# Kernel tuning notes

Hardware: AMD Instinct MI355X
Metric: run time of the kernel (lower is better)

Reference implementation:

```python
import jax, jax.numpy as jnp
import numpy as np

DN = ('NCHW', 'OIHW', 'NCHW')


def conv2d(x, w, b, pad=1):
    y = jax.lax.conv_general_dilated(x, w, window_strides=(1, 1),
                                     padding=[(pad, pad), (pad, pad)],
                                     dimension_numbers=DN)
    return y + b[None, :, None, None]


def deform_conv2d(x, offset, w, b):
    """Deformable conv v1 (torchvision layout): offset [B, 2*K*K, H, W],
    channel 2k = dy_k, 2k+1 = dx_k, kernel points row-major."""
    B, C, H, W = x.shape
    K = 3
    off = offset.reshape(B, K * K, 2, H, W)
    dy, dx = off[:, :, 0], off[:, :, 1]            # [B,9,H,W]
    ky = jnp.repeat(jnp.arange(K) - 1, K).astype(x.dtype)   # row-major kernel grid
    kx = jnp.tile(jnp.arange(K) - 1, K).astype(x.dtype)
    hh = jnp.arange(H, dtype=x.dtype)
    ww = jnp.arange(W, dtype=x.dtype)
    py = hh[None, None, :, None] + ky[None, :, None, None] + dy  # [B,9,H,W]
    px = ww[None, None, None, :] + kx[None, :, None, None] + dx

    y0 = jnp.floor(py)
    x0 = jnp.floor(px)
    ly, lx = py - y0, px - x0
    y0i, x0i = y0.astype(jnp.int32), x0.astype(jnp.int32)

    def gather(yi, xi):
        valid = ((yi >= 0) & (yi < H) & (xi >= 0) & (xi < W))
        yc = jnp.clip(yi, 0, H - 1)
        xc = jnp.clip(xi, 0, W - 1)
        # per-batch fancy gather: [C,H,W] indexed by [9,H,W] -> [C,9,H,W]
        g = jax.vmap(lambda xb, yy, xx: xb[:, yy, xx])(x, yc, xc)  # [B,C,9,H,W]
        return g * valid[:, None].astype(x.dtype)

    w00 = ((1 - ly) * (1 - lx))[:, None]
    w01 = ((1 - ly) * lx)[:, None]
    w10 = (ly * (1 - lx))[:, None]
    w11 = (ly * lx)[:, None]
    val = (gather(y0i, x0i) * w00 + gather(y0i, x0i + 1) * w01 +
           gather(y0i + 1, x0i) * w10 + gather(y0i + 1, x0i + 1) * w11)  # [B,C,9,H,W]

    wk = w.reshape(w.shape[0], C * K * K)                 # [Cout, C*9]
    out = jnp.einsum('bkhw,ok->bohw', val.reshape(B, C * K * K, H, W), wk)
    return out + b[None, :, None, None]


def setup_inputs() -> dict:
    key = jax.random.key(0)
    k1, k2, k3, k4 = jax.random.split(key, 4)
    B, Cin, Cout, H, W = 8, 128, 256, 64, 64
    fan = 1.0 / np.sqrt(Cin * 9)
    return {
        'x': jax.random.normal(k1, (B, Cin, H, W), jnp.float32),
        'w_off': jax.random.normal(k2, (18, Cin, 3, 3), jnp.float32) * 0.01,
        'b_off': jnp.zeros((18,), jnp.float32),
        'w_def': jax.random.normal(k3, (Cout, Cin, 3, 3), jnp.float32) * fan,
        'b_def': jax.random.normal(k4, (Cout,), jnp.float32) * 0.01,
    }


def reference(x, w_off, b_off, w_def, b_def):
    offset = conv2d(x, w_off, b_off, pad=1)
    y = deform_conv2d(x, offset, w_def, b_def)
    return jax.nn.relu(y)
```

## Files before the change

### kernel.cpp

```cpp
#include <hip/hip_runtime.h>
#include <hip/hip_bf16.h>

#define HH 64
#define WW 64
#define CIN 128
#define COUT 256
#define KK 1152
#define TP 32
#define PW 66
#define XTIMG (PW*PW*CIN)

typedef short bf16x8 __attribute__((ext_vector_type(8)));
typedef float f32x4  __attribute__((ext_vector_type(4)));

__device__ inline short f2bf(float f) {
    union { float f; unsigned u; } v; v.f = f;
    unsigned r = v.u + 0x7FFFu + ((v.u >> 16) & 1u);
    return (short)(r >> 16);
}
__device__ inline float bf2f(ushort u) {
    union { unsigned u; float f; } v; v.u = (unsigned)u << 16; return v.f;
}

__global__ __launch_bounds__(256) void transpose_x(const float* __restrict__ x,
                                                   ushort* __restrict__ xt) {
    __shared__ short tl[64][130];
    int hp = blockIdx.x;
    int b  = blockIdx.y;
    int t  = threadIdx.x;
    ushort* row = xt + ((size_t)b * PW + hp) * PW * CIN;
    if (hp == 0 || hp == PW - 1) {
        for (int i = 0; i < 33; i++) row[i * 256 + t] = 0;
        return;
    }
    int h = hp - 1;
    int w = t & 63, cq = t >> 6;
    for (int it = 0; it < 32; it++) {
        int c = it * 4 + cq;
        tl[w][c] = f2bf(x[(((size_t)b * CIN + c) << 12) + (h << 6) + w]);
    }
    __syncthreads();
    for (int it = 0; it < 33; it++) {
        int flat = it * 256 + t;
        int wp = flat >> 7, c = flat & 127;
        ushort v = (wp == 0 || wp == PW - 1) ? (ushort)0 : (ushort)tl[wp - 1][c];
        row[flat] = v;
    }
}

__global__ void cast_wf(const float* __restrict__ wd, short* __restrict__ wf) {
    int ks = blockIdx.x, m = blockIdx.y, l = threadIdx.x;
    int co = m * 16 + (l & 15);
    bf16x8 v;
#pragma unroll
    for (int j = 0; j < 8; j++) {
        int ckp = ks * 32 + ((l >> 4) << 3) + j;
        int c = ckp & 127, k = ckp >> 7;
        v[j] = f2bf(wd[(size_t)co * KK + c * 9 + k]);
    }
    *(bf16x8*)(wf + ((size_t)(m * 36 + ks) * 64 + l) * 8) = v;
}

__global__ void cast_wfo(const float* __restrict__ w, short* __restrict__ wfo) {
    int ks = blockIdx.x, m = blockIdx.y, l = threadIdx.x;
    int co = m * 16 + (l & 15);
    bf16x8 v;
#pragma unroll
    for (int j = 0; j < 8; j++) {
        int ckp = ks * 32 + ((l >> 4) << 3) + j;
        int c = ckp & 127, k = ckp >> 7;
        v[j] = (co < 18) ? f2bf(w[(size_t)co * KK + c * 9 + k]) : (short)0;
    }
    *(bf16x8*)(wfo + ((size_t)(m * 36 + ks) * 64 + l) * 8) = v;
}

__global__ __launch_bounds__(256, 4) void off_mfma(const ushort* __restrict__ xt,
                                                   const short* __restrict__ wfo,
                                                   const float* __restrict__ bo,
                                                   float* __restrict__ off) {
    __shared__ short s_val[2][TP][128];

    int t = threadIdx.x, bi = blockIdx.x;
    int b = bi & 7, h = (bi >> 3) & 63, tile = bi >> 9, w0 = tile * TP;
    const ushort* xb = xt + (size_t)b * XTIMG;

    bf16x8 r0, r1;
    int cpix = t >> 3;
    int g0 = ((2 * t) & 15), g1 = g0 + 1;
    int gs0 = (g0 ^ (cpix & 15)) * 8, gs1 = (g1 ^ (cpix & 15)) * 8;

    auto oload = [&](int k) {
        const ushort* base = xb + ((size_t)(h + k / 3) * PW + w0 + k % 3) * CIN;
        r0 = *(const bf16x8*)(base + t * 16);
        r1 = *(const bf16x8*)(base + t * 16 + 8);
    };
    auto ostore = [&](int buf) {
        *(bf16x8*)&s_val[buf][cpix][gs0] = r0;
        *(bf16x8*)&s_val[buf][cpix][gs1] = r1;
    };

    int wv = t >> 6, l = t & 63, lane16 = l & 15, quad = l >> 4;
    int mt = wv >> 1, nt = wv & 1;
    f32x4 acc = {0.f, 0.f, 0.f, 0.f};
    const short* Ab = wfo + (size_t)l * 8 + (size_t)mt * 36 * 512;

    oload(0); ostore(0);
    __syncthreads();
    for (int k = 0; k < 9; k++) {
        if (k < 8) oload(k + 1);
#pragma unroll
        for (int ksp = 0; ksp < 4; ksp++) {
            int ks = k * 4 + ksp;
            bf16x8 a  = *(const bf16x8*)(Ab + ks * 512);
            bf16x8 bf = *(const bf16x8*)&s_val[k & 1][nt * 16 + lane16][((ksp * 4 + quad) ^ lane16) * 8];
            acc = __builtin_amdgcn_mfma_f32_16x16x32_bf16(a, bf, acc, 0, 0, 0);
        }
        if (k < 8) ostore((k + 1) & 1);
        __syncthreads();
    }
    int cob = mt * 16 + quad * 4;
#pragma unroll
    for (int r = 0; r < 4; r++) {
        int co = cob + r;
        if (co < 18)
            off[(((size_t)b * 18 + co) << 12) + (h << 6) + w0 + nt * 16 + lane16] = acc[r] + bo[co];
    }
}

__global__ __launch_bounds__(256, 4) void deform_mfma(const ushort* __restrict__ xt,
                                                      const float* __restrict__ off,
                                                      const short* __restrict__ wf,
                                                      const float* __restrict__ bias,
                                                      float* __restrict__ out) {
    __shared__ float4  s_w[9][TP];
    __shared__ ushort2 s_o[9][TP];
    __shared__ short   s_val[2][TP][128];

    int t = threadIdx.x, bi = blockIdx.x;
    int b = bi & 7, h = (bi >> 3) & 63, tile = bi >> 9, w0 = tile * TP;

    for (int jj = t; jj < 9 * TP; jj += 256) {
        int k = jj >> 5, pixj = jj & 31, wp = w0 + pixj;
        float dy = off[(((size_t)b * 18 + 2 * k    ) << 12) + (h << 6) + wp];
        float dx = off[(((size_t)b * 18 + 2 * k + 1) << 12) + (h << 6) + wp];
        float py = (float)(h + k / 3 - 1) + dy;
        float px = (float)(wp + k % 3 - 1) + dx;
        float y0f = floorf(py), x0f = floorf(px);
        float ly = py - y0f, lx = px - x0f;
        int y0 = (int)y0f, x0 = (int)x0f;
        float a0, a1;
        if (x0 >= 0 && x0 <= 62)      { a0 = 1.f - lx; a1 = lx; }
        else if (x0 == -1)            { a0 = lx;       a1 = 0.f; }
        else if (x0 == 63)            { a0 = 0.f;      a1 = 1.f - lx; }
        else                          { a0 = 0.f;      a1 = 0.f; }
        int xb0 = min(max(x0, 0), 62);
        bool vy0 = (y0 >= 0) && (y0 < HH);
        bool vy1 = (y0 >= -1) && (y0 < HH - 1);
        int y0c = min(max(y0, 0), HH - 1);
        int y1c = min(max(y0 + 1, 0), HH - 1);
        float wy0 = (1.f - ly) * (vy0 ? 1.f : 0.f);
        float wy1 = ly * (vy1 ? 1.f : 0.f);
        s_o[k][pixj] = make_ushort2((ushort)((y0c + 1) * PW + xb0 + 1),
                                    (ushort)((y1c + 1) * PW + xb0 + 1));
        s_w[k][pixj] = make_float4(wy0 * a0, wy0 * a1, wy1 * a0, wy1 * a1);
    }
    __syncthreads();

    int pix = t & 31, cs = t >> 5, pm = pix & 15;
    const ushort* xb = xt + (size_t)b * XTIMG;
    int gs0 = ((cs * 2) ^ pm) * 8, gs1 = ((cs * 2 + 1) ^ pm) * 8;

    bf16x8 r[8];
    auto gload = [&](int k) {
        ushort2 o = s_o[k][pix];
        const ushort* p0 = xb + (size_t)o.x * CIN + cs * 16;
        const ushort* p1 = xb + (size_t)o.y * CIN + cs * 16;
        r[0] = *(const bf16x8*)(p0);       r[1] = *(const bf16x8*)(p0 + 8);
        r[2] = *(const bf16x8*)(p0 + 128); r[3] = *(const bf16x8*)(p0 + 136);
        r[4] = *(const bf16x8*)(p1);       r[5] = *(const bf16x8*)(p1 + 8);
        r[6] = *(const bf16x8*)(p1 + 128); r[7] = *(const bf16x8*)(p1 + 136);
    };
    auto gstore = [&](int k, int buf) {
        float4 w4 = s_w[k][pix];
        bf16x8 va, vb;
#pragma unroll
        for (int j = 0; j < 8; j++) {
            float v = w4.x * bf2f((ushort)r[0][j]) + w4.y * bf2f((ushort)r[2][j])
                    + w4.z * bf2f((ushort)r[4][j]) + w4.w * bf2f((ushort)r[6][j]);
            float u = w4.x * bf2f((ushort)r[1][j]) + w4.y * bf2f((ushort)r[3][j])
                    + w4.z * bf2f((ushort)r[5][j]) + w4.w * bf2f((ushort)r[7][j]);
            va[j] = f2bf(v);
            vb[j] = f2bf(u);
        }
        *(bf16x8*)&s_val[buf][pix][gs0] = va;
        *(bf16x8*)&s_val[buf][pix][gs1] = vb;
    };

    int wv = t >> 6, l = t & 63, lane16 = l & 15, quad = l >> 4;
    f32x4 z = {0.f, 0.f, 0.f, 0.f};
    f32x4 acc[4][2];
#pragma unroll
    for (int i = 0; i < 4; i++)
#pragma unroll
        for (int j = 0; j < 2; j++) acc[i][j] = z;

    const short* Ab = wf + (size_t)l * 8 + (size_t)(wv * 4) * 36 * 512;

    gload(0); gstore(0, 0);
    __syncthreads();
    for (int k = 0; k < 9; k++) {
        if (k < 8) gload(k + 1);
#pragma unroll
        for (int ksp = 0; ksp < 4; ksp++) {
            int ks = k * 4 + ksp;
            bf16x8 a0 = *(const bf16x8*)(Ab + (0 * 36 + ks) * 512);
            bf16x8 a1 = *(const bf16x8*)(Ab + (1 * 36 + ks) * 512);
            bf16x8 a2 = *(const bf16x8*)(Ab + (2 * 36 + ks) * 512);
            bf16x8 a3 = *(const bf16x8*)(Ab + (3 * 36 + ks) * 512);
            int gsw = ((ksp * 4 + quad) ^ lane16) * 8;
            bf16x8 b0 = *(const bf16x8*)&s_val[k & 1][lane16     ][gsw];
            bf16x8 b1 = *(const bf16x8*)&s_val[k & 1][16 + lane16][gsw];
            acc[0][0] = __builtin_amdgcn_mfma_f32_16x16x32_bf16(a0, b0, acc[0][0], 0, 0, 0);
            acc[1][0] = __builtin_amdgcn_mfma_f32_16x16x32_bf16(a1, b0, acc[1][0], 0, 0, 0);
            acc[2][0] = __builtin_amdgcn_mfma_f32_16x16x32_bf16(a2, b0, acc[2][0], 0, 0, 0);
            acc[3][0] = __builtin_amdgcn_mfma_f32_16x16x32_bf16(a3, b0, acc[3][0], 0, 0, 0);
            acc[0][1] = __builtin_amdgcn_mfma_f32_16x16x32_bf16(a0, b1, acc[0][1], 0, 0, 0);
            acc[1][1] = __builtin_amdgcn_mfma_f32_16x16x32_bf16(a1, b1, acc[1][1], 0, 0, 0);
            acc[2][1] = __builtin_amdgcn_mfma_f32_16x16x32_bf16(a2, b1, acc[2][1], 0, 0, 0);
            acc[3][1] = __builtin_amdgcn_mfma_f32_16x16x32_bf16(a3, b1, acc[3][1], 0, 0, 0);
        }
        if (k < 8) gstore(k + 1, (k + 1) & 1);
        __syncthreads();
    }

#pragma unroll
    for (int ct = 0; ct < 4; ct++) {
        int co = wv * 64 + ct * 16 + quad * 4;
#pragma unroll
        for (int pt = 0; pt < 2; pt++) {
            int colx = w0 + pt * 16 + lane16;
#pragma unroll
            for (int rr = 0; rr < 4; rr++) {
                float v = acc[ct][pt][rr] + bias[co + rr];
                out[(((size_t)b * COUT + co + rr) << 12) + (h << 6) + colx] = fmaxf(v, 0.f);
            }
        }
    }
}

extern "C" void kernel_launch(void* const* d_in, const int* in_sizes, int n_in,
                              void* d_out, int out_size, void* d_ws, size_t ws_size,
                              hipStream_t stream) {
    const float* x     = (const float*)d_in[0];
    const float* w_off = (const float*)d_in[1];
    const float* b_off = (const float*)d_in[2];
    const float* w_def = (const float*)d_in[3];
    const float* b_def = (const float*)d_in[4];
    float* out = (float*)d_out;

    float*  offset = (float*)d_ws;
    short*  wf     = (short*)(offset + (size_t)8 * 18 * HH * WW);
    short*  wfo    = wf + (size_t)16 * 36 * 512;
    ushort* xt     = (ushort*)(wfo + (size_t)2 * 36 * 512);

    transpose_x<<<dim3(PW, 8), 256, 0, stream>>>(x, xt);
    cast_wf<<<dim3(36, 16), 64, 0, stream>>>(w_def, wf);
    cast_wfo<<<dim3(36, 2), 64, 0, stream>>>(w_off, wfo);
    off_mfma<<<1024, 256, 0, stream>>>(xt, wfo, b_off, offset);
    deform_mfma<<<1024, 256, 0, stream>>>(xt, offset, wf, b_def, out);
}
```

Baseline: 147.7 us.

## Fuse offset conv into deform kernel, restage gathers via LDS, vectorize transpose

The offset convolution and the deformable conv now run in one kernel: offsets go to shared memory instead of global, and the two weight cast kernels merge into one launch. The deform gather is reorganised so that 4 threads load one corner row into a raw LDS buffer, and a separate combine pass does the bilinear blend. The transpose kernel uses float4 loads and ushort4 stores. This removes the offset round-trip through global memory and two launches. In exchange it uses much more LDS (occupancy bound drops to 3), adds extra barriers per k step, and drops the double-buffering of the value tile.

```diff
diff --git a/kernel.cpp b/kernel.cpp
--- a/kernel.cpp
+++ b/kernel.cpp
@@ -9,6 +9,7 @@
 #define TP 32
 #define PW 66
 #define XTIMG (PW*PW*CIN)
+#define RS 264
 
 typedef short bf16x8 __attribute__((ext_vector_type(8)));
 typedef float f32x4  __attribute__((ext_vector_type(4)));
@@ -24,125 +25,129 @@
 
 __global__ __launch_bounds__(256) void transpose_x(const float* __restrict__ x,
                                                    ushort* __restrict__ xt) {
-    __shared__ short tl[64][130];
     int hp = blockIdx.x;
     int b  = blockIdx.y;
     int t  = threadIdx.x;
     ushort* row = xt + ((size_t)b * PW + hp) * PW * CIN;
     if (hp == 0 || hp == PW - 1) {
-        for (int i = 0; i < 33; i++) row[i * 256 + t] = 0;
+        ushort4 z4 = {0, 0, 0, 0};
+        for (int f = t; f < 2112; f += 256) ((ushort4*)row)[f] = z4;
         return;
     }
+    __shared__ short tl[66 * 132];
     int h = hp - 1;
-    int w = t & 63, cq = t >> 6;
-    for (int it = 0; it < 32; it++) {
-        int c = it * 4 + cq;
-        tl[w][c] = f2bf(x[(((size_t)b * CIN + c) << 12) + (h << 6) + w]);
-    }
-    __syncthreads();
-    for (int it = 0; it < 33; it++) {
-        int flat = it * 256 + t;
-        int wp = flat >> 7, c = flat & 127;
-        ushort v = (wp == 0 || wp == PW - 1) ? (ushort)0 : (ushort)tl[wp - 1][c];
-        row[flat] = v;
-    }
-}
-
-__global__ void cast_wf(const float* __restrict__ wd, short* __restrict__ wf) {
+    if (t < 128) { tl[t] = 0; tl[65 * 132 + t] = 0; }
+    const float* xbh = x + (((size_t)b * CIN) << 12) + (h << 6);
+#pragma unroll
+    for (int it = 0; it < 8; it++) {
+        int c  = it * 16 + (t >> 4);
+        int w4 = (t & 15) * 4;
+        float4 v = *(const float4*)(xbh + ((size_t)c << 12) + w4);
+        tl[(w4 + 1) * 132 + c] = f2bf(v.x);
+        tl[(w4 + 2) * 132 + c] = f2bf(v.y);
+        tl[(w4 + 3) * 132 + c] = f2bf(v.z);
+        tl[(w4 + 4) * 132 + c] = f2bf(v.w);
+    }
+    __syncthreads();
+    for (int f = t; f < 2112; f += 256) {
+        int wp = f >> 5, c4 = (f & 31) * 4;
+        const short* s = &tl[wp * 132 + c4];
+        ushort4 v; v.x = s[0]; v.y = s[1]; v.z = s[2]; v.w = s[3];
+        ((ushort4*)row)[f] = v;
+    }
+}
+
+__global__ void cast_wall(const float* __restrict__ wd, const float* __restrict__ wo,
+                          short* __restrict__ wf, short* __restrict__ wfo) {
     int ks = blockIdx.x, m = blockIdx.y, l = threadIdx.x;
-    int co = m * 16 + (l & 15);
     bf16x8 v;
-#pragma unroll
-    for (int j = 0; j < 8; j++) {
-        int ckp = ks * 32 + ((l >> 4) << 3) + j;
-        int c = ckp & 127, k = ckp >> 7;
-        v[j] = f2bf(wd[(size_t)co * KK + c * 9 + k]);
-    }
-    *(bf16x8*)(wf + ((size_t)(m * 36 + ks) * 64 + l) * 8) = v;
-}
-
-__global__ void cast_wfo(const float* __restrict__ w, short* __restrict__ wfo) {
-    int ks = blockIdx.x, m = blockIdx.y, l = threadIdx.x;
-    int co = m * 16 + (l & 15);
-    bf16x8 v;
-#pragma unroll
-    for (int j = 0; j < 8; j++) {
-        int ckp = ks * 32 + ((l >> 4) << 3) + j;
-        int c = ckp & 127, k = ckp >> 7;
-        v[j] = (co < 18) ? f2bf(w[(size_t)co * KK + c * 9 + k]) : (short)0;
-    }
-    *(bf16x8*)(wfo + ((size_t)(m * 36 + ks) * 64 + l) * 8) = v;
-}
-
-__global__ __launch_bounds__(256, 4) void off_mfma(const ushort* __restrict__ xt,
-                                                   const short* __restrict__ wfo,
-                                                   const float* __restrict__ bo,
-                                                   float* __restrict__ off) {
-    __shared__ short s_val[2][TP][128];
+    if (m < 16) {
+        int co = m * 16 + (l & 15);
+#pragma unroll
+        for (int j = 0; j < 8; j++) {
+            int ckp = ks * 32 + ((l >> 4) << 3) + j;
+            int c = ckp & 127, k = ckp >> 7;
+            v[j] = f2bf(wd[(size_t)co * KK + c * 9 + k]);
+        }
+        *(bf16x8*)(wf + ((size_t)(m * 36 + ks) * 64 + l) * 8) = v;
+    } else {
+        int mm = m - 16;
+        int co = mm * 16 + (l & 15);
+#pragma unroll
+        for (int j = 0; j < 8; j++) {
+            int ckp = ks * 32 + ((l >> 4) << 3) + j;
+            int c = ckp & 127, k = ckp >> 7;
+            v[j] = (co < 18) ? f2bf(wo[(size_t)co * KK + c * 9 + k]) : (short)0;
+        }
+        *(bf16x8*)(wfo + ((size_t)(mm * 36 + ks) * 64 + l) * 8) = v;
+    }
+}
+
+__global__ __launch_bounds__(256, 3) void fused_deform(const ushort* __restrict__ xt,
+                                                       const short* __restrict__ wf,
+                                                       const short* __restrict__ wfo,
+                                                       const float* __restrict__ bo,
+                                                       const float* __restrict__ bias,
+                                                       float* __restrict__ out) {
+    __shared__ short   s_raw[64 * RS];
+    __shared__ short   s_val[TP][128];
+    __shared__ float   s_off[18][TP];
+    __shared__ float4  s_w[9][TP];
+    __shared__ ushort2 s_o[9][TP];
 
     int t = threadIdx.x, bi = blockIdx.x;
     int b = bi & 7, h = (bi >> 3) & 63, tile = bi >> 9, w0 = tile * TP;
     const ushort* xb = xt + (size_t)b * XTIMG;
-
-    bf16x8 r0, r1;
-    int cpix = t >> 3;
-    int g0 = ((2 * t) & 15), g1 = g0 + 1;
-    int gs0 = (g0 ^ (cpix & 15)) * 8, gs1 = (g1 ^ (cpix & 15)) * 8;
-
-    auto oload = [&](int k) {
-        const ushort* base = xb + ((size_t)(h + k / 3) * PW + w0 + k % 3) * CIN;
-        r0 = *(const bf16x8*)(base + t * 16);
-        r1 = *(const bf16x8*)(base + t * 16 + 8);
-    };
-    auto ostore = [&](int buf) {
-        *(bf16x8*)&s_val[buf][cpix][gs0] = r0;
-        *(bf16x8*)&s_val[buf][cpix][gs1] = r1;
-    };
-
     int wv = t >> 6, l = t & 63, lane16 = l & 15, quad = l >> 4;
-    int mt = wv >> 1, nt = wv & 1;
-    f32x4 acc = {0.f, 0.f, 0.f, 0.f};
-    const short* Ab = wfo + (size_t)l * 8 + (size_t)mt * 36 * 512;
-
-    oload(0); ostore(0);
-    __syncthreads();
-    for (int k = 0; k < 9; k++) {
-        if (k < 8) oload(k + 1);
-#pragma unroll
-        for (int ksp = 0; ksp < 4; ksp++) {
-            int ks = k * 4 + ksp;
-            bf16x8 a  = *(const bf16x8*)(Ab + ks * 512);
-            bf16x8 bf = *(const bf16x8*)&s_val[k & 1][nt * 16 + lane16][((ksp * 4 + quad) ^ lane16) * 8];
-            acc = __builtin_amdgcn_mfma_f32_16x16x32_bf16(a, bf, acc, 0, 0, 0);
-        }
-        if (k < 8) ostore((k + 1) & 1);
+
+    {
+        short* sv0 = s_raw;
+        short* sv1 = s_raw + 4096;
+        int cpix = t >> 3;
+        int g0 = 2 * (t & 7), g1 = g0 + 1;
+        int gs0 = (g0 ^ (cpix & 15)) * 8, gs1 = (g1 ^ (cpix & 15)) * 8;
+        bf16x8 r0, r1;
+        auto oload = [&](int k) {
+            const ushort* base = xb + ((size_t)(h + k / 3) * PW + w0 + k % 3) * CIN;
+            r0 = *(const bf16x8*)(base + t * 16);
+            r1 = *(const bf16x8*)(base + t * 16 + 8);
+        };
+        auto ostore = [&](int buf) {
+            short* sv = buf ? sv1 : sv0;
+            *(bf16x8*)(sv + cpix * 128 + gs0) = r0;
+            *(bf16x8*)(sv + cpix * 128 + gs1) = r1;
+        };
+        int mt = wv >> 1, nt = wv & 1;
+        f32x4 aoff = {0.f, 0.f, 0.f, 0.f};
+        const short* Ab = wfo + (size_t)l * 8 + (size_t)mt * 36 * 512;
+
+        oload(0); ostore(0);
         __syncthreads();
-    }
-    int cob = mt * 16 + quad * 4;
-#pragma unroll
-    for (int r = 0; r < 4; r++) {
-        int co = cob + r;
-        if (co < 18)
-            off[(((size_t)b * 18 + co) << 12) + (h << 6) + w0 + nt * 16 + lane16] = acc[r] + bo[co];
-    }
-}
-
-__global__ __launch_bounds__(256, 4) void deform_mfma(const ushort* __restrict__ xt,
-                                                      const float* __restrict__ off,
-                                                      const short* __restrict__ wf,
-                                                      const float* __restrict__ bias,
-                                                      float* __restrict__ out) {
-    __shared__ float4  s_w[9][TP];
-    __shared__ ushort2 s_o[9][TP];
-    __shared__ short   s_val[2][TP][128];
-
-    int t = threadIdx.x, bi = blockIdx.x;
-    int b = bi & 7, h = (bi >> 3) & 63, tile = bi >> 9, w0 = tile * TP;
+        for (int k = 0; k < 9; k++) {
+            if (k < 8) oload(k + 1);
+            const short* sv = (k & 1) ? sv1 : sv0;
+#pragma unroll
+            for (int ksp = 0; ksp < 4; ksp++) {
+                bf16x8 a  = *(const bf16x8*)(Ab + (k * 4 + ksp) * 512);
+                bf16x8 bf = *(const bf16x8*)(sv + (nt * 16 + lane16) * 128 + ((ksp * 4 + quad) ^ lane16) * 8);
+                aoff = __builtin_amdgcn_mfma_f32_16x16x32_bf16(a, bf, aoff, 0, 0, 0);
+            }
+            if (k < 8) ostore((k + 1) & 1);
+            __syncthreads();
+        }
+        int cob = mt * 16 + quad * 4;
+#pragma unroll
+        for (int r = 0; r < 4; r++) {
+            int co = cob + r;
+            if (co < 18) s_off[co][nt * 16 + lane16] = aoff[r] + bo[co];
+        }
+    }
+    __syncthreads();
 
     for (int jj = t; jj < 9 * TP; jj += 256) {
         int k = jj >> 5, pixj = jj & 31, wp = w0 + pixj;
-        float dy = off[(((size_t)b * 18 + 2 * k    ) << 12) + (h << 6) + wp];
-        float dx = off[(((size_t)b * 18 + 2 * k + 1) << 12) + (h << 6) + wp];
+        float dy = s_off[2 * k][pixj];
+        float dx = s_off[2 * k + 1][pixj];
         float py = (float)(h + k / 3 - 1) + dy;
         float px = (float)(wp + k % 3 - 1) + dx;
         float y0f = floorf(py), x0f = floorf(px);
@@ -166,60 +171,70 @@
     }
     __syncthreads();
 
-    int pix = t & 31, cs = t >> 5, pm = pix & 15;
-    const ushort* xb = xt + (size_t)b * XTIMG;
-    int gs0 = ((cs * 2) ^ pm) * 8, gs1 = ((cs * 2 + 1) ^ pm) * 8;
-
-    bf16x8 r[8];
+    int g = t >> 2, sub = t & 3;
+    int gpix = g & 31, gr = g >> 5;
+    bf16x8 rv[8];
     auto gload = [&](int k) {
-        ushort2 o = s_o[k][pix];
-        const ushort* p0 = xb + (size_t)o.x * CIN + cs * 16;
-        const ushort* p1 = xb + (size_t)o.y * CIN + cs * 16;
-        r[0] = *(const bf16x8*)(p0);       r[1] = *(const bf16x8*)(p0 + 8);
-        r[2] = *(const bf16x8*)(p0 + 128); r[3] = *(const bf16x8*)(p0 + 136);
-        r[4] = *(const bf16x8*)(p1);       r[5] = *(const bf16x8*)(p1 + 8);
-        r[6] = *(const bf16x8*)(p1 + 128); r[7] = *(const bf16x8*)(p1 + 136);
+        ushort2 o = s_o[k][gpix];
+        int loc = gr ? o.y : o.x;
+        const ushort* p = xb + (size_t)loc * CIN + sub * 8;
+#pragma unroll
+        for (int i = 0; i < 8; i++) rv[i] = *(const bf16x8*)(p + i * 32);
     };
-    auto gstore = [&](int k, int buf) {
-        float4 w4 = s_w[k][pix];
-        bf16x8 va, vb;
-#pragma unroll
-        for (int j = 0; j < 8; j++) {
-            float v = w4.x * bf2f((ushort)r[0][j]) + w4.y * bf2f((ushort)r[2][j])
-                    + w4.z * bf2f((ushort)r[4][j]) + w4.w * bf2f((ushort)r[6][j]);
-            float u = w4.x * bf2f((ushort)r[1][j]) + w4.y * bf2f((ushort)r[3][j])
-                    + w4.z * bf2f((ushort)r[5][j]) + w4.w * bf2f((ushort)r[7][j]);
-            va[j] = f2bf(v);
-            vb[j] = f2bf(u);
-        }
-        *(bf16x8*)&s_val[buf][pix][gs0] = va;
-        *(bf16x8*)&s_val[buf][pix][gs1] = vb;
+    auto gstore = [&]() {
+        short* d = s_raw + g * RS + sub * 8;
+#pragma unroll
+        for (int i = 0; i < 8; i++) *(bf16x8*)(d + i * 32) = rv[i];
     };
-
-    int wv = t >> 6, l = t & 63, lane16 = l & 15, quad = l >> 4;
+    int cpix2 = t & 31, cg = t >> 5;
+    auto combine = [&](int k) {
+        float4 w4 = s_w[k][cpix2];
+        const short* r0b = s_raw + cpix2 * RS;
+        const short* r1b = s_raw + (cpix2 + 32) * RS;
+#pragma unroll
+        for (int j2 = 0; j2 < 2; j2++) {
+            int ch = cg * 16 + j2 * 8;
+            bf16x8 c00 = *(const bf16x8*)(r0b + ch);
+            bf16x8 c01 = *(const bf16x8*)(r0b + 128 + ch);
+            bf16x8 c10 = *(const bf16x8*)(r1b + ch);
+            bf16x8 c11 = *(const bf16x8*)(r1b + 128 + ch);
+            bf16x8 fr;
+#pragma unroll
+            for (int i = 0; i < 8; i++) {
+                float v = w4.x * bf2f((ushort)c00[i]) + w4.y * bf2f((ushort)c01[i])
+                        + w4.z * bf2f((ushort)c10[i]) + w4.w * bf2f((ushort)c11[i]);
+                fr[i] = f2bf(v);
+            }
+            *(bf16x8*)&s_val[cpix2][((cg * 2 + j2) ^ (cpix2 & 15)) * 8] = fr;
+        }
+    };
+
     f32x4 z = {0.f, 0.f, 0.f, 0.f};
     f32x4 acc[4][2];
 #pragma unroll
     for (int i = 0; i < 4; i++)
 #pragma unroll
         for (int j = 0; j < 2; j++) acc[i][j] = z;
-
-    const short* Ab = wf + (size_t)l * 8 + (size_t)(wv * 4) * 36 * 512;
-
-    gload(0); gstore(0, 0);
-    __syncthreads();
+    const short* Aw = wf + (size_t)l * 8;
+
+    gload(0);
+    gstore();
+    __syncthreads();
+    combine(0);
+    gload(1);
+    __syncthreads();
+
     for (int k = 0; k < 9; k++) {
-        if (k < 8) gload(k + 1);
 #pragma unroll
         for (int ksp = 0; ksp < 4; ksp++) {
             int ks = k * 4 + ksp;
-            bf16x8 a0 = *(const bf16x8*)(Ab + (0 * 36 + ks) * 512);
-            bf16x8 a1 = *(const bf16x8*)(Ab + (1 * 36 + ks) * 512);
-            bf16x8 a2 = *(const bf16x8*)(Ab + (2 * 36 + ks) * 512);
-            bf16x8 a3 = *(const bf16x8*)(Ab + (3 * 36 + ks) * 512);
             int gsw = ((ksp * 4 + quad) ^ lane16) * 8;
-            bf16x8 b0 = *(const bf16x8*)&s_val[k & 1][lane16     ][gsw];
-            bf16x8 b1 = *(const bf16x8*)&s_val[k & 1][16 + lane16][gsw];
+            bf16x8 b0 = *(const bf16x8*)&s_val[lane16     ][gsw];
+            bf16x8 b1 = *(const bf16x8*)&s_val[16 + lane16][gsw];
+            bf16x8 a0 = *(const bf16x8*)(Aw + (size_t)((wv * 4 + 0) * 36 + ks) * 512);
+            bf16x8 a1 = *(const bf16x8*)(Aw + (size_t)((wv * 4 + 1) * 36 + ks) * 512);
+            bf16x8 a2 = *(const bf16x8*)(Aw + (size_t)((wv * 4 + 2) * 36 + ks) * 512);
+            bf16x8 a3 = *(const bf16x8*)(Aw + (size_t)((wv * 4 + 3) * 36 + ks) * 512);
             acc[0][0] = __builtin_amdgcn_mfma_f32_16x16x32_bf16(a0, b0, acc[0][0], 0, 0, 0);
             acc[1][0] = __builtin_amdgcn_mfma_f32_16x16x32_bf16(a1, b0, acc[1][0], 0, 0, 0);
             acc[2][0] = __builtin_amdgcn_mfma_f32_16x16x32_bf16(a2, b0, acc[2][0], 0, 0, 0);
@@ -229,8 +244,13 @@
             acc[2][1] = __builtin_amdgcn_mfma_f32_16x16x32_bf16(a2, b1, acc[2][1], 0, 0, 0);
             acc[3][1] = __builtin_amdgcn_mfma_f32_16x16x32_bf16(a3, b1, acc[3][1], 0, 0, 0);
         }
-        if (k < 8) gstore(k + 1, (k + 1) & 1);
-        __syncthreads();
+        if (k < 8) {
+            gstore();
+            __syncthreads();
+            combine(k + 1);
+            if (k < 7) gload(k + 2);
+            __syncthreads();
+        }
     }
 
 #pragma unroll
@@ -258,14 +278,11 @@
     const float* b_def = (const float*)d_in[4];
     float* out = (float*)d_out;
 
-    float*  offset = (float*)d_ws;
-    short*  wf     = (short*)(offset + (size_t)8 * 18 * HH * WW);
-    short*  wfo    = wf + (size_t)16 * 36 * 512;
-    ushort* xt     = (ushort*)(wfo + (size_t)2 * 36 * 512);
+    short*  wf  = (short*)d_ws;
+    short*  wfo = wf + (size_t)16 * 36 * 512;
+    ushort* xt  = (ushort*)(wfo + (size_t)2 * 36 * 512);
 
     transpose_x<<<dim3(PW, 8), 256, 0, stream>>>(x, xt);
-    cast_wf<<<dim3(36, 16), 64, 0, stream>>>(w_def, wf);
-    cast_wfo<<<dim3(36, 2), 64, 0, stream>>>(w_off, wfo);
-    off_mfma<<<1024, 256, 0, stream>>>(xt, wfo, b_off, offset);
-    deform_mfma<<<1024, 256, 0, stream>>>(xt, offset, wf, b_def, out);
-}
+    cast_wall<<<dim3(36, 18), 64, 0, stream>>>(w_def, w_off, wf, wfo);
+    fused_deform<<<1024, 256, 0, stream>>>(xt, wf, wfo, b_off, b_def, out);
+}
```

Measured after the change: 135.3 us. 1.09x faster.
